# Performance work log

Hardware: AMD Instinct MI355X
Metric: run time of the kernel (lower is better)

## Reference

```python
import jax, jax.numpy as jnp
import numpy as np

B, S, D_X, D_H = 1024, 512, 128, 128
A_VOCAB, A_EMB, T_VOCAB, T_EMB = 100, 32, 4, 16
GRU_IN = D_X + A_EMB + T_EMB + 1  # 177
Y_IN = D_H + D_X + A_EMB + T_EMB  # 304


def _lin_init(key, d_in, d_out):
    k1, k2 = jax.random.split(key)
    lim = 1.0 / np.sqrt(d_in)
    W = jax.random.uniform(k1, (d_out, d_in), minval=-lim, maxval=lim, dtype=jnp.float32)
    b = jax.random.uniform(k2, (d_out,), minval=-lim, maxval=lim, dtype=jnp.float32)
    return W, b


def setup_inputs() -> dict:
    key = jax.random.key(0)
    ks = jax.random.split(key, 16)
    x = jax.random.normal(ks[0], (B, D_X), dtype=jnp.float32)
    a = jax.random.randint(ks[1], (B, S), 0, A_VOCAB)
    t = jax.random.randint(ks[2], (B, S), 0, T_VOCAB)
    y = jax.random.uniform(ks[3], (B, S), dtype=jnp.float32)
    mask = jnp.ones((B, S), dtype=jnp.float32)

    xW, xb = _lin_init(ks[4], D_X, D_X)                 # x_proj
    a_emb = jax.random.normal(ks[5], (A_VOCAB, A_EMB), dtype=jnp.float32)
    t_emb = jax.random.normal(ks[6], (T_VOCAB, T_EMB), dtype=jnp.float32)
    W_ih, b_ih = _lin_init(ks[7], GRU_IN, 3 * D_H)      # GRUCell input weights
    W_hh, b_hh = _lin_init(ks[8], D_H, 3 * D_H)         # GRUCell hidden weights
    h0W, h0b = _lin_init(ks[9], D_X, D_H)               # h0 MLP
    tW1, tb1 = _lin_init(ks[10], D_H, D_H)              # t_head
    tW2, tb2 = _lin_init(ks[11], D_H, T_VOCAB)
    yW1, yb1 = _lin_init(ks[12], Y_IN, D_H)             # y_head
    yW2, yb2 = _lin_init(ks[13], D_H, 1)
    return {
        'x': x, 'a': a, 't': t, 'y': y, 'mask': mask,
        'xW': xW, 'xb': xb, 'a_emb': a_emb, 't_emb': t_emb,
        'W_ih': W_ih, 'b_ih': b_ih, 'W_hh': W_hh, 'b_hh': b_hh,
        'h0W': h0W, 'h0b': h0b,
        'tW1': tW1, 'tb1': tb1, 'tW2': tW2, 'tb2': tb2,
        'yW1': yW1, 'yb1': yb1, 'yW2': yW2, 'yb2': yb2,
    }


def _crn_forward(x, y, mask, xW, xb, a_emb, t_emb, W_ih, b_ih, W_hh, b_hh,
                 h0W, h0b, tW1, tb1, tW2, tb2, yW1, yb1, yW2, yb2, a, t):
    gelu = lambda v: jax.nn.gelu(v, approximate=False)
    x_enc = x @ xW.T + xb                       # [B, D_X]
    h = jnp.tanh(x_enc @ h0W.T + h0b)           # [B, D_H]
    a_e = a_emb[a]                              # [B, S, A_EMB]
    t_e = t_emb[t]                              # [B, S, T_EMB]
    y3 = y[..., None]                           # [B, S, 1]

    # time-major slices for scan
    a_e_t = jnp.swapaxes(a_e, 0, 1)
    t_e_t = jnp.swapaxes(t_e, 0, 1)
    y_t = jnp.swapaxes(y3, 0, 1)
    m_t = jnp.swapaxes(mask, 0, 1)[..., None]   # [S, B, 1]

    def step(h, inp):
        ae, te, yt, m = inp
        # grad_reverse is identity in forward; dropout off (eval)
        t_logits = gelu(h @ tW1.T + tb1) @ tW2.T + tb2          # [B, T_VOCAB]
        y_in = jnp.concatenate([h, x_enc, ae, te], axis=-1)
        y_logits = gelu(y_in @ yW1.T + yb1) @ yW2.T + yb2        # [B, 1]
        upd = jnp.concatenate([x_enc, ae, te, yt], axis=-1)      # [B, GRU_IN]
        gx = upd @ W_ih.T + b_ih
        gh = h @ W_hh.T + b_hh
        r = jax.nn.sigmoid(gx[:, :D_H] + gh[:, :D_H])
        z = jax.nn.sigmoid(gx[:, D_H:2 * D_H] + gh[:, D_H:2 * D_H])
        n = jnp.tanh(gx[:, 2 * D_H:] + r * gh[:, 2 * D_H:])
        h_next = (1.0 - z) * n + z * h
        h_new = m * h_next + (1.0 - m) * h
        return h_new, (y_logits, t_logits, h)

    _, (y_seq, t_seq, h_seq) = jax.lax.scan(step, h, (a_e_t, t_e_t, y_t, m_t))
    # back to batch-major [B, S, ...]
    return (jnp.swapaxes(y_seq, 0, 1), jnp.swapaxes(t_seq, 0, 1), jnp.swapaxes(h_seq, 0, 1))


def reference(x, a, t, y, mask, xW, xb, a_emb, t_emb, W_ih, b_ih, W_hh, b_hh,
              h0W, h0b, tW1, tb1, tW2, tb2, yW1, yb1, yW2, yb2):
    return _crn_forward(x, y, mask, xW, xb, a_emb, t_emb, W_ih, b_ih, W_hh, b_hh,
                        h0W, h0b, tW1, tb1, tW2, tb2, yW1, yb1, yW2, yb2, a, t)
```

## Files before the change

### kernel.cpp

```cpp
#include <hip/hip_runtime.h>
#include <math.h>

#define SLEN 512

typedef _Float16 half8 __attribute__((ext_vector_type(8)));
typedef _Float16 half2v __attribute__((ext_vector_type(2)));
typedef __fp16 fp16x2 __attribute__((ext_vector_type(2)));
typedef float f32x4 __attribute__((ext_vector_type(4)));
typedef unsigned int uint;

union U4H8 { uint4 u; half8 h; };
union UH2 { uint u; half2v v; fp16x2 p; };

static __device__ __forceinline__ uint packh2(float a, float b){
  UH2 x; x.p = __builtin_amdgcn_cvt_pkrtz(a, b); return x.u;
}
static __device__ __forceinline__ float loh(uint u){ UH2 x; x.u=u; return (float)x.v[0]; }
static __device__ __forceinline__ float hih(uint u){ UH2 x; x.u=u; return (float)x.v[1]; }
static __device__ __forceinline__ half8 ld_h8(const uint* p){
  U4H8 x; x.u = *(const uint4*)p; return x.h;
}
static __device__ __forceinline__ float rcpf(float x){ return __builtin_amdgcn_rcpf(x); }
static __device__ __forceinline__ float sigm(float v){ return rcpf(1.0f+__expf(-v)); }
static __device__ __forceinline__ float tanh_f(float v){ return 1.0f - 2.0f*rcpf(__expf(2.0f*v)+1.0f); }
static __device__ __forceinline__ float gelu_exact(float v){
  return 0.5f*v*(1.0f+erff(v*0.7071067811865475f));
}
#define MFMA(a,b,c) __builtin_amdgcn_mfma_f32_16x16x32_f16((a),(b),(c),0,0,0)

static __device__ __forceinline__ void wg_barrier(){
  __builtin_amdgcn_sched_barrier(0);
  asm volatile("s_waitcnt lgkmcnt(0)" ::: "memory");
  __builtin_amdgcn_s_barrier();
  __builtin_amdgcn_sched_barrier(0);
}

__global__ void k_sample(const float* __restrict__ x, const float* __restrict__ xW, const float* __restrict__ xb,
                         const float* __restrict__ h0W, const float* __restrict__ h0b,
                         const float* __restrict__ W_ih, const float* __restrict__ b_ih, const float* __restrict__ b_hh,
                         const float* __restrict__ yW1, const float* __restrict__ yb1,
                         float* __restrict__ w_h0, float* __restrict__ w_xgx, float* __restrict__ w_yx)
{
  const int b = blockIdx.x, tid = threadIdx.x;
  __shared__ float sx[128];
  __shared__ float sxe[128];
  if (tid < 128) sx[tid] = x[b*128+tid];
  __syncthreads();
  if (tid < 128) {
    float acc = xb[tid];
    #pragma unroll 8
    for (int j=0;j<128;++j) acc += xW[tid*128+j]*sx[j];
    sxe[tid] = acc;
  }
  __syncthreads();
  {
    const int o = tid;
    float acc = b_ih[o] + (o < 256 ? b_hh[o] : 0.f);
    #pragma unroll 8
    for (int j=0;j<128;++j) acc += W_ih[o*177+j]*sxe[j];
    w_xgx[b*384+o] = acc;
  }
  if (tid < 128) {
    float acc = h0b[tid];
    #pragma unroll 8
    for (int j=0;j<128;++j) acc += h0W[tid*128+j]*sxe[j];
    w_h0[b*128+tid] = tanhf(acc);
    float a2 = yb1[tid];
    #pragma unroll 8
    for (int j=0;j<128;++j) a2 += yW1[tid*304+128+j]*sxe[j];
    w_yx[b*128+tid] = a2;
  }
}

__global__ __launch_bounds__(384,1) void k_recur(
  const float* __restrict__ W_hh, const float* __restrict__ W_ih, const float* __restrict__ b_hh,
  const int* __restrict__ a, const int* __restrict__ tt,
  const float* __restrict__ yy, const float* __restrict__ mask,
  const float* __restrict__ w_h0, const float* __restrict__ w_xgx,
  const float* __restrict__ a_emb, const float* __restrict__ t_emb,
  float* __restrict__ o_h, uint* __restrict__ h16)
{
  const int tid = threadIdx.x;
  const int wv = tid>>6, lane = tid&63, q = lane>>4, c = lane&15;
  const int g = wv>>1, H = wv&1;
  const int b0 = blockIdx.x*16;
  const int rowbase = g*128 + H*64;

  __shared__ __align__(16) uint s_h[2][16*68];
  __shared__ __align__(16) uint s_ext[2][16*36];
  __shared__ __align__(16) uint s_rz[2][1024];
  __shared__ __align__(16) uint s_chunk[2][1024];
  __shared__ __align__(16) uint s_al[1600];
  __shared__ __align__(16) uint s_te[32];

  half8 wf[24];
  #pragma unroll
  for (int t4=0;t4<4;++t4) {
    const int row = rowbase + t4*16 + c;
    #pragma unroll
    for (int kt=0;kt<4;++kt) {
      const float4* wp = (const float4*)(W_hh + row*128 + kt*32 + q*8);
      float4 v0 = wp[0], v1 = wp[1];
      half8 hv;
      hv[0]=(_Float16)v0.x; hv[1]=(_Float16)v0.y; hv[2]=(_Float16)v0.z; hv[3]=(_Float16)v0.w;
      hv[4]=(_Float16)v1.x; hv[5]=(_Float16)v1.y; hv[6]=(_Float16)v1.z; hv[7]=(_Float16)v1.w;
      wf[t4*6+kt] = hv;
    }
    #pragma unroll
    for (int kt=4;kt<6;++kt) {
      half8 hv;
      #pragma unroll
      for (int j=0;j<8;++j) {
        int k2 = (kt-4)*32 + q*8 + j;
        float v = (k2 < 49) ? W_ih[row*177 + 128 + k2] : 0.f;
        hv[j] = (_Float16)v;
      }
      wf[t4*6+kt] = hv;
    }
  }
  f32x4 xg[4];
  #pragma unroll
  for (int t4=0;t4<4;++t4)
    #pragma unroll
    for (int r=0;r<4;++r)
      xg[t4][r] = w_xgx[(b0+c)*384 + rowbase + t4*16 + q*4 + r];
  f32x4 bhh[4]; float hm[16];
  if (g==2) {
    #pragma unroll
    for (int t4=0;t4<4;++t4)
      #pragma unroll
      for (int r=0;r<4;++r) {
        bhh[t4][r] = b_hh[256 + H*64 + t4*16 + q*4 + r];
        hm[t4*4+r] = w_h0[(b0+c)*128 + H*64 + t4*16 + q*4 + r];
      }
  }
  for (int d = tid; d < 1600; d += 384) {
    int row = d>>4, col = d&15;
    s_al[d] = packh2(a_emb[row*32+2*col], a_emb[row*32+2*col+1]);
  }
  if (tid < 32) {
    int row = tid>>3, col = tid&7;
    s_te[tid] = packh2(t_emb[row*16+2*col], t_emb[row*16+2*col+1]);
  }
  uint4 cr0, cr1, cr2, cr3;
  if (wv==0) {
    const uint* bp = (q==0) ? (const uint*)a : (q==1) ? (const uint*)tt
                   : (q==2) ? (const uint*)yy : (const uint*)mask;
    const uint4* p = (const uint4*)(bp + (size_t)(b0+c)*512);
    cr0=p[0]; cr1=p[1]; cr2=p[2]; cr3=p[3];
    uint4* dst = (uint4*)&s_chunk[0][q*256 + c*16];
    dst[0]=cr0; dst[1]=cr1; dst[2]=cr2; dst[3]=cr3;
  }
  if (g==2) {
    #pragma unroll
    for (int t4=0;t4<4;++t4) {
      int base = c*68 + H*32 + t4*8 + q*2;
      s_h[0][base]   = packh2(hm[t4*4+0], hm[t4*4+1]);
      s_h[0][base+1] = packh2(hm[t4*4+2], hm[t4*4+3]);
    }
  }
  __syncthreads();
  if (g==0) {
    int av = (int)s_chunk[0][c*16];
    int tv = (int)s_chunk[0][256 + c*16];
    uint yu = s_chunk[0][512 + c*16];
    float yv = __uint_as_float(yu);
    #pragma unroll
    for (int i=0;i<4;++i) {
      int d = H*16 + q*4 + i;
      uint u;
      if (d < 16) u = s_al[av*16 + d];
      else if (d < 24) u = s_te[tv*8 + (d-16)];
      else if (d == 24) u = packh2(yv, 0.f);
      else u = 0u;
      s_ext[0][c*36 + d] = u;
    }
  }
  __syncthreads();

  f32x4 acc[4], acc2[4];

  for (int s=0; s<SLEN; ++s) {
    const int pb = s&1;
    half8 hb[4], eb[2];
    #pragma unroll
    for (int kt=0;kt<4;++kt) hb[kt] = ld_h8(&s_h[pb][c*68 + kt*16 + q*4]);
    #pragma unroll
    for (int e=0;e<2;++e)    eb[e]  = ld_h8(&s_ext[pb][c*36 + e*16 + q*4]);

    if (g < 2) {
      if (g==1 && s>0) {
        const int ob = (s-1)&1;
        const int smp = H*8 + (lane>>3), ch = lane&7;
        const uint* hp = &s_h[ob][smp*68 + ch*8];
        const size_t pr = (size_t)(b0+smp)*SLEN + (s-1);
        if (h16) {
          uint4* hq = (uint4*)(h16 + pr*64 + ch*8);
          hq[0] = *(const uint4*)(hp);
          hq[1] = *(const uint4*)(hp + 4);
        } else {
          float* op = o_h + pr*128 + ch*16;
          #pragma unroll
          for (int i2=0;i2<2;++i2) {
            uint4 u = *(const uint4*)(hp + i2*4);
            float4 f0 = make_float4(loh(u.x), hih(u.x), loh(u.y), hih(u.y));
            float4 f1 = make_float4(loh(u.z), hih(u.z), loh(u.w), hih(u.w));
            *(float4*)(op + i2*8)     = f0;
            *(float4*)(op + i2*8 + 4) = f1;
          }
        }
      }
      #pragma unroll
      for (int t4=0;t4<4;++t4) acc[t4] = xg[t4];
      #pragma unroll
      for (int kt=0;kt<6;++kt) {
        half8 bsel = (kt<4) ? hb[kt] : eb[kt-4];
        #pragma unroll
        for (int t4=0;t4<4;++t4) acc[t4] = MFMA(wf[t4*6+kt], bsel, acc[t4]);
      }
      #pragma unroll
      for (int t4=0;t4<4;++t4)
        #pragma unroll
        for (int pr=0;pr<2;++pr) {
          float s0 = sigm(acc[t4][2*pr]), s1 = sigm(acc[t4][2*pr+1]);
          s_rz[g][(((H*4+t4)*2+pr)*4+q)*16 + c] = packh2(s0, s1);
        }
      if (wv==0) {
        if ((s&15)==8 && s<490) {
          const int s0n = ((s>>4)+1)*16;
          const uint* bp = (q==0) ? (const uint*)a : (q==1) ? (const uint*)tt
                         : (q==2) ? (const uint*)yy : (const uint*)mask;
          const uint4* p = (const uint4*)(bp + (size_t)(b0+c)*512 + s0n);
          cr0=p[0]; cr1=p[1]; cr2=p[2]; cr3=p[3];
        }
        if ((s&15)==9 && s<491) {
          uint4* dst = (uint4*)&s_chunk[((s>>4)+1)&1][q*256 + c*16];
          dst[0]=cr0; dst[1]=cr1; dst[2]=cr2; dst[3]=cr3;
        }
      }
    } else {
      #pragma unroll
      for (int t4=0;t4<4;++t4) { acc[t4] = bhh[t4]; acc2[t4] = xg[t4]; }
      #pragma unroll
      for (int kt=0;kt<4;++kt)
        #pragma unroll
        for (int t4=0;t4<4;++t4) acc[t4] = MFMA(wf[t4*6+kt], hb[kt], acc[t4]);
      #pragma unroll
      for (int kt=4;kt<6;++kt)
        #pragma unroll
        for (int t4=0;t4<4;++t4) acc2[t4] = MFMA(wf[t4*6+kt], eb[kt-4], acc2[t4]);
    }
    wg_barrier();
    if (g==2) {
      const float mval = __uint_as_float(s_chunk[(s>>4)&1][768 + c*16 + (s&15)]);
      #pragma unroll
      for (int t4=0;t4<4;++t4)
        #pragma unroll
        for (int pr=0;pr<2;++pr) {
          const int slot = (((H*4+t4)*2+pr)*4+q)*16 + c;
          uint ru = s_rz[0][slot], zu = s_rz[1][slot];
          const int i0 = t4*4 + 2*pr;
          float n0 = tanh_f(acc2[t4][2*pr]   + loh(ru)*acc[t4][2*pr]);
          float n1 = tanh_f(acc2[t4][2*pr+1] + hih(ru)*acc[t4][2*pr+1]);
          float h0o = hm[i0], h1o = hm[i0+1];
          float hn0 = n0 + loh(zu)*(h0o - n0);
          float hn1 = n1 + hih(zu)*(h1o - n1);
          hm[i0]   = h0o + mval*(hn0 - h0o);
          hm[i0+1] = h1o + mval*(hn1 - h1o);
        }
      const int nb = (s+1)&1;
      #pragma unroll
      for (int t4=0;t4<4;++t4) {
        int base = c*68 + H*32 + t4*8 + q*2;
        s_h[nb][base]   = packh2(hm[t4*4+0], hm[t4*4+1]);
        s_h[nb][base+1] = packh2(hm[t4*4+2], hm[t4*4+3]);
      }
    } else if (g==0 && s < SLEN-1) {
      const int sn = s+1;
      const int par2 = (sn>>4)&1, st = sn&15;
      int av = (int)s_chunk[par2][c*16 + st];
      int tv = (int)s_chunk[par2][256 + c*16 + st];
      float yv = __uint_as_float(s_chunk[par2][512 + c*16 + st]);
      #pragma unroll
      for (int i=0;i<4;++i) {
        int d = H*16 + q*4 + i;
        uint u;
        if (d < 16) u = s_al[av*16 + d];
        else if (d < 24) u = s_te[tv*8 + (d-16)];
        else if (d == 24) u = packh2(yv, 0.f);
        else u = 0u;
        s_ext[(s+1)&1][c*36 + d] = u;
      }
    }
    wg_barrier();
  }
  if (g==1) {
    const int ob = (SLEN-1)&1;
    const int smp = H*8 + (lane>>3), ch = lane&7;
    const uint* hp = &s_h[ob][smp*68 + ch*8];
    const size_t pr = (size_t)(b0+smp)*SLEN + (SLEN-1);
    if (h16) {
      uint4* hq = (uint4*)(h16 + pr*64 + ch*8);
      hq[0] = *(const uint4*)(hp);
      hq[1] = *(const uint4*)(hp + 4);
    } else {
      float* op = o_h + pr*128 + ch*16;
      #pragma unroll
      for (int i2=0;i2<2;++i2) {
        uint4 u = *(const uint4*)(hp + i2*4);
        float4 f0 = make_float4(loh(u.x), hih(u.x), loh(u.y), hih(u.y));
        float4 f1 = make_float4(loh(u.z), hih(u.z), loh(u.w), hih(u.w));
        *(float4*)(op + i2*8)     = f0;
        *(float4*)(op + i2*8 + 4) = f1;
      }
    }
  }
}

template<bool H16>
__global__ __launch_bounds__(256,2) void k_heads(
  const float* __restrict__ tW1, const float* __restrict__ tb1,
  const float* __restrict__ tW2, const float* __restrict__ tb2,
  const float* __restrict__ yW1, const float* __restrict__ yW2, const float* __restrict__ yb2,
  const int* __restrict__ a, const int* __restrict__ tt,
  const float* __restrict__ w_yx,
  const float* __restrict__ a_emb, const float* __restrict__ t_emb,
  const float* __restrict__ h_f32, const uint* __restrict__ h16,
  float* __restrict__ o_y, float* __restrict__ o_t, float* __restrict__ o_h)
{
  const int tid = threadIdx.x;
  const int wv = tid>>6, lane = tid&63, q = lane>>4, c = lane&15;
  const bool isY = (wv >= 2);
  const int uh = wv&1;
  const int pair = wv>>1;
  const int p0 = blockIdx.x*1024;
  const int b0 = blockIdx.x*2;

  __shared__ __align__(16) uint s_al[100*20];
  __shared__ __align__(16) uint s_te[32];
  __shared__ __align__(16) uint s_gb[2][2][16*68];

  for (int d = tid; d < 1600; d += 256) {
    int row = d>>4, col = d&15;
    s_al[row*20+col] = packh2(a_emb[row*32+2*col], a_emb[row*32+2*col+1]);
  }
  if (tid < 32) {
    int row = tid>>3, col = tid&7;
    s_te[row*8+col] = packh2(t_emb[row*16+2*col], t_emb[row*16+2*col+1]);
  }

  half8 wf[24];
  const float* W1 = isY ? yW1 : tW1;
  const int w1stride = isY ? 304 : 128;
  #pragma unroll
  for (int ut=0;ut<4;++ut) {
    const int unit = uh*64 + ut*16 + c;
    #pragma unroll
    for (int kt=0;kt<4;++kt) {
      const float4* wp = (const float4*)(W1 + unit*w1stride + kt*32 + q*8);
      float4 v0 = wp[0], v1 = wp[1];
      half8 hv;
      hv[0]=(_Float16)v0.x; hv[1]=(_Float16)v0.y; hv[2]=(_Float16)v0.z; hv[3]=(_Float16)v0.w;
      hv[4]=(_Float16)v1.x; hv[5]=(_Float16)v1.y; hv[6]=(_Float16)v1.z; hv[7]=(_Float16)v1.w;
      wf[ut*6+kt] = hv;
    }
    #pragma unroll
    for (int kt=4;kt<6;++kt) {
      half8 hv;
      #pragma unroll
      for (int j=0;j<8;++j) {
        int k2 = (kt-4)*32 + q*8 + j;
        float v = (isY && k2 < 48) ? yW1[unit*304 + 256 + k2] : 0.f;
        hv[j] = (_Float16)v;
      }
      wf[ut*6+kt] = hv;
    }
  }
  half8 w2f[4];
  #pragma unroll
  for (int kt=0;kt<4;++kt) {
    half8 hv;
    #pragma unroll
    for (int j=0;j<8;++j) {
      float v = 0.f;
      if (!isY && c < 4) v = tW2[c*128 + kt*32 + q*8 + j];
      if ( isY && c == 0) v = yW2[kt*32 + q*8 + j];
      hv[j] = (_Float16)v;
    }
    w2f[kt] = hv;
  }
  float tb2r[4]; float yb2s = yb2[0];
  #pragma unroll
  for (int r=0;r<4;++r) tb2r[r] = tb2[r];

  __syncthreads();

  #pragma unroll 1
  for (int bh=0; bh<2; ++bh) {
    f32x4 bsr[4];
    #pragma unroll
    for (int ut=0;ut<4;++ut)
      #pragma unroll
      for (int r=0;r<4;++r)
        bsr[ut][r] = isY ? w_yx[(b0+bh)*128 + uh*64 + ut*16 + q*4 + r]
                         : tb1[uh*64 + ut*16 + q*4 + r];

    #pragma unroll 1
    for (int ti=0; ti<32; ++ti) {
      const int tile = bh*32 + ti;
      const int par = ti&1;
      const int p = p0 + tile*16 + c;

      half8 hb[4];
      if (H16) {
        const uint* hp = h16 + (size_t)p*64;
        #pragma unroll
        for (int kt=0;kt<4;++kt) hb[kt] = ld_h8(hp + kt*16 + q*4);
      } else {
        const float* hp = h_f32 + (size_t)p*128;
        #pragma unroll
        for (int kt=0;kt<4;++kt) {
          const float4* fp = (const float4*)(hp + kt*32 + q*8);
          float4 v0 = fp[0], v1 = fp[1];
          half8 hv;
          hv[0]=(_Float16)v0.x; hv[1]=(_Float16)v0.y; hv[2]=(_Float16)v0.z; hv[3]=(_Float16)v0.w;
          hv[4]=(_Float16)v1.x; hv[5]=(_Float16)v1.y; hv[6]=(_Float16)v1.z; hv[7]=(_Float16)v1.w;
          hb[kt] = hv;
        }
      }
      if (H16 && !isY) {
        float* op = o_h + (size_t)p*128;
        #pragma unroll
        for (int kk=0;kk<2;++kk) {
          const int kt = uh*2 + kk;
          float4 f0 = make_float4((float)hb[kt][0], (float)hb[kt][1], (float)hb[kt][2], (float)hb[kt][3]);
          float4 f1 = make_float4((float)hb[kt][4], (float)hb[kt][5], (float)hb[kt][6], (float)hb[kt][7]);
          *(float4*)(op + kt*32 + q*8)     = f0;
          *(float4*)(op + kt*32 + q*8 + 4) = f1;
        }
      }

      f32x4 acc[4];
      #pragma unroll
      for (int ut=0;ut<4;++ut) acc[ut] = bsr[ut];
      #pragma unroll
      for (int kt=0;kt<4;++kt)
        #pragma unroll
        for (int ut=0;ut<4;++ut) acc[ut] = MFMA(wf[ut*6+kt], hb[kt], acc[ut]);
      if (isY) {
        half8 eb[2];
        const int av = a[p], tv = tt[p];
        eb[0] = ld_h8(&s_al[av*20 + q*4]);
        if (q < 2) eb[1] = ld_h8(&s_te[tv*8 + q*4]);
        else {
          half8 z;
          #pragma unroll
          for (int j=0;j<8;++j) z[j] = (_Float16)0.f;
          eb[1] = z;
        }
        #pragma unroll
        for (int kt=4;kt<6;++kt)
          #pragma unroll
          for (int ut=0;ut<4;++ut) acc[ut] = MFMA(wf[ut*6+kt], eb[kt-4], acc[ut]);
      }

      #pragma unroll
      for (int ut=0;ut<4;++ut)
        #pragma unroll
        for (int pr=0;pr<2;++pr) {
          float g0 = gelu_exact(acc[ut][2*pr]);
          float g1 = gelu_exact(acc[ut][2*pr+1]);
          s_gb[pair][par][c*68 + uh*32 + ut*8 + 2*q + pr] = packh2(g0, g1);
        }
      wg_barrier();

      f32x4 a2; a2[0]=0.f; a2[1]=0.f; a2[2]=0.f; a2[3]=0.f;
      #pragma unroll
      for (int kt=0;kt<4;++kt) {
        half8 gb = ld_h8(&s_gb[pair][par][c*68 + kt*16 + q*4]);
        a2 = MFMA(w2f[kt], gb, a2);
      }
      if (uh==0 && lane < 16) {
        if (!isY) {
          float4 o = make_float4(a2[0]+tb2r[0], a2[1]+tb2r[1], a2[2]+tb2r[2], a2[3]+tb2r[3]);
          *(float4*)&o_t[(size_t)p*4] = o;
        } else {
          o_y[p] = a2[0] + yb2s;
        }
      }
    }
  }
}

extern "C" void kernel_launch(void* const* d_in, const int* in_sizes, int n_in,
                              void* d_out, int out_size, void* d_ws, size_t ws_size,
                              hipStream_t stream) {
  (void)in_sizes; (void)n_in; (void)out_size;
  const float* x     = (const float*)d_in[0];
  const int*   a     = (const int*)  d_in[1];
  const int*   tt    = (const int*)  d_in[2];
  const float* y     = (const float*)d_in[3];
  const float* mask  = (const float*)d_in[4];
  const float* xW    = (const float*)d_in[5];
  const float* xb    = (const float*)d_in[6];
  const float* a_emb = (const float*)d_in[7];
  const float* t_emb = (const float*)d_in[8];
  const float* W_ih  = (const float*)d_in[9];
  const float* b_ih  = (const float*)d_in[10];
  const float* W_hh  = (const float*)d_in[11];
  const float* b_hh  = (const float*)d_in[12];
  const float* h0W   = (const float*)d_in[13];
  const float* h0b   = (const float*)d_in[14];
  const float* tW1   = (const float*)d_in[15];
  const float* tb1   = (const float*)d_in[16];
  const float* tW2   = (const float*)d_in[17];
  const float* tb2   = (const float*)d_in[18];
  const float* yW1   = (const float*)d_in[19];
  const float* yb1   = (const float*)d_in[20];
  const float* yW2   = (const float*)d_in[21];
  const float* yb2   = (const float*)d_in[22];

  float* o_y = (float*)d_out;
  float* o_t = o_y + 524288;
  float* o_h = o_y + 2621440;

  float* ws    = (float*)d_ws;
  float* w_h0  = ws;
  float* w_xgx = ws + 131072;
  float* w_yx  = ws + 524288;

  const size_t H16_BYTES = (size_t)524288 * 256;
  uint* h16 = nullptr;
  if (ws_size >= (size_t)655360*4 + H16_BYTES) h16 = (uint*)(ws + 655360);

  k_sample<<<1024, 384, 0, stream>>>(x, xW, xb, h0W, h0b, W_ih, b_ih, b_hh, yW1, yb1,
                                     w_h0, w_xgx, w_yx);
  k_recur<<<64, 384, 0, stream>>>(W_hh, W_ih, b_hh, a, tt, y, mask,
                                  w_h0, w_xgx, a_emb, t_emb, o_h, h16);
  if (h16)
    k_heads<true><<<512, 256, 0, stream>>>(tW1, tb1, tW2, tb2, yW1, yW2, yb2, a, tt,
                                           w_yx, a_emb, t_emb, o_h, h16, o_y, o_t, o_h);
  else
    k_heads<false><<<512, 256, 0, stream>>>(tW1, tb1, tW2, tb2, yW1, yW2, yb2, a, tt,
                                            w_yx, a_emb, t_emb, o_h, nullptr, o_y, o_t, o_h);
}
```

Measured before the change: 1.354 ms.

## Restructure GRU recurrence to 8 waves owning all gates per row slice

The recurrent kernel now uses 8 waves, each computing the r, z and n gates for its own 16 hidden units. This removes the cross-wave exchange of r/z through shared memory and drops one of the two workgroup barriers per timestep. Each wave also builds its own embedding input and writes h directly, instead of having dedicated waves prepare the input and store h. The heads kernel is flattened into a single 64-tile loop that prefetches the next tile's h and indices, and the second-layer work alternates between wave halves. The costs are more waves per block and duplicated embedding loads in every wave.

```diff
diff --git a/kernel.cpp b/kernel.cpp
--- a/kernel.cpp
+++ b/kernel.cpp
@@ -28,11 +28,9 @@
 }
 #define MFMA(a,b,c) __builtin_amdgcn_mfma_f32_16x16x32_f16((a),(b),(c),0,0,0)
 
-static __device__ __forceinline__ void wg_barrier(){
-  __builtin_amdgcn_sched_barrier(0);
+static __device__ __forceinline__ void wg_sync(){
   asm volatile("s_waitcnt lgkmcnt(0)" ::: "memory");
   __builtin_amdgcn_s_barrier();
-  __builtin_amdgcn_sched_barrier(0);
 }
 
 __global__ void k_sample(const float* __restrict__ x, const float* __restrict__ xW, const float* __restrict__ xb,
@@ -72,7 +70,7 @@
   }
 }
 
-__global__ __launch_bounds__(384,1) void k_recur(
+__global__ __launch_bounds__(512,1) void k_recur(
   const float* __restrict__ W_hh, const float* __restrict__ W_ih, const float* __restrict__ b_hh,
   const int* __restrict__ a, const int* __restrict__ tt,
   const float* __restrict__ yy, const float* __restrict__ mask,
@@ -82,32 +80,29 @@
 {
   const int tid = threadIdx.x;
   const int wv = tid>>6, lane = tid&63, q = lane>>4, c = lane&15;
-  const int g = wv>>1, H = wv&1;
   const int b0 = blockIdx.x*16;
-  const int rowbase = g*128 + H*64;
+  const int r0 = wv*16;
 
   __shared__ __align__(16) uint s_h[2][16*68];
-  __shared__ __align__(16) uint s_ext[2][16*36];
-  __shared__ __align__(16) uint s_rz[2][1024];
   __shared__ __align__(16) uint s_chunk[2][1024];
   __shared__ __align__(16) uint s_al[1600];
   __shared__ __align__(16) uint s_te[32];
 
-  half8 wf[24];
-  #pragma unroll
-  for (int t4=0;t4<4;++t4) {
-    const int row = rowbase + t4*16 + c;
-    #pragma unroll
-    for (int kt=0;kt<4;++kt) {
+  half8 wf[18];
+  #pragma unroll
+  for (int g=0; g<3; ++g) {
+    const int row = g*128 + r0 + c;
+    #pragma unroll
+    for (int kt=0; kt<4; ++kt) {
       const float4* wp = (const float4*)(W_hh + row*128 + kt*32 + q*8);
       float4 v0 = wp[0], v1 = wp[1];
       half8 hv;
       hv[0]=(_Float16)v0.x; hv[1]=(_Float16)v0.y; hv[2]=(_Float16)v0.z; hv[3]=(_Float16)v0.w;
       hv[4]=(_Float16)v1.x; hv[5]=(_Float16)v1.y; hv[6]=(_Float16)v1.z; hv[7]=(_Float16)v1.w;
-      wf[t4*6+kt] = hv;
-    }
-    #pragma unroll
-    for (int kt=4;kt<6;++kt) {
+      wf[g*6+kt] = hv;
+    }
+    #pragma unroll
+    for (int kt=4; kt<6; ++kt) {
       half8 hv;
       #pragma unroll
       for (int j=0;j<8;++j) {
@@ -115,26 +110,20 @@
         float v = (k2 < 49) ? W_ih[row*177 + 128 + k2] : 0.f;
         hv[j] = (_Float16)v;
       }
-      wf[t4*6+kt] = hv;
-    }
-  }
-  f32x4 xg[4];
-  #pragma unroll
-  for (int t4=0;t4<4;++t4)
-    #pragma unroll
-    for (int r=0;r<4;++r)
-      xg[t4][r] = w_xgx[(b0+c)*384 + rowbase + t4*16 + q*4 + r];
-  f32x4 bhh[4]; float hm[16];
-  if (g==2) {
-    #pragma unroll
-    for (int t4=0;t4<4;++t4)
-      #pragma unroll
-      for (int r=0;r<4;++r) {
-        bhh[t4][r] = b_hh[256 + H*64 + t4*16 + q*4 + r];
-        hm[t4*4+r] = w_h0[(b0+c)*128 + H*64 + t4*16 + q*4 + r];
-      }
-  }
-  for (int d = tid; d < 1600; d += 384) {
+      wf[g*6+kt] = hv;
+    }
+  }
+  f32x4 xgr, xgz, xgn, bhh, hm;
+  #pragma unroll
+  for (int j=0;j<4;++j) {
+    const int rr = r0 + q*4 + j;
+    xgr[j] = w_xgx[(b0+c)*384 +       rr];
+    xgz[j] = w_xgx[(b0+c)*384 + 128 + rr];
+    xgn[j] = w_xgx[(b0+c)*384 + 256 + rr];
+    bhh[j] = b_hh[256 + rr];
+    hm[j]  = w_h0[(b0+c)*128 + rr];
+  }
+  for (int d = tid; d < 1600; d += 512) {
     int row = d>>4, col = d&15;
     s_al[d] = packh2(a_emb[row*32+2*col], a_emb[row*32+2*col+1]);
   }
@@ -151,169 +140,66 @@
     uint4* dst = (uint4*)&s_chunk[0][q*256 + c*16];
     dst[0]=cr0; dst[1]=cr1; dst[2]=cr2; dst[3]=cr3;
   }
-  if (g==2) {
-    #pragma unroll
-    for (int t4=0;t4<4;++t4) {
-      int base = c*68 + H*32 + t4*8 + q*2;
-      s_h[0][base]   = packh2(hm[t4*4+0], hm[t4*4+1]);
-      s_h[0][base+1] = packh2(hm[t4*4+2], hm[t4*4+3]);
-    }
-  }
+  s_h[0][c*68 + wv*8 + q*2]     = packh2(hm[0], hm[1]);
+  s_h[0][c*68 + wv*8 + q*2 + 1] = packh2(hm[2], hm[3]);
   __syncthreads();
-  if (g==0) {
-    int av = (int)s_chunk[0][c*16];
-    int tv = (int)s_chunk[0][256 + c*16];
-    uint yu = s_chunk[0][512 + c*16];
-    float yv = __uint_as_float(yu);
-    #pragma unroll
-    for (int i=0;i<4;++i) {
-      int d = H*16 + q*4 + i;
-      uint u;
-      if (d < 16) u = s_al[av*16 + d];
-      else if (d < 24) u = s_te[tv*8 + (d-16)];
-      else if (d == 24) u = packh2(yv, 0.f);
-      else u = 0u;
-      s_ext[0][c*36 + d] = u;
-    }
-  }
-  __syncthreads();
-
-  f32x4 acc[4], acc2[4];
 
   for (int s=0; s<SLEN; ++s) {
-    const int pb = s&1;
-    half8 hb[4], eb[2];
+    const int pb = s&1, par = (s>>4)&1, st = s&15;
+    half8 hb[4];
     #pragma unroll
     for (int kt=0;kt<4;++kt) hb[kt] = ld_h8(&s_h[pb][c*68 + kt*16 + q*4]);
-    #pragma unroll
-    for (int e=0;e<2;++e)    eb[e]  = ld_h8(&s_ext[pb][c*36 + e*16 + q*4]);
-
-    if (g < 2) {
-      if (g==1 && s>0) {
-        const int ob = (s-1)&1;
-        const int smp = H*8 + (lane>>3), ch = lane&7;
-        const uint* hp = &s_h[ob][smp*68 + ch*8];
-        const size_t pr = (size_t)(b0+smp)*SLEN + (s-1);
-        if (h16) {
-          uint4* hq = (uint4*)(h16 + pr*64 + ch*8);
-          hq[0] = *(const uint4*)(hp);
-          hq[1] = *(const uint4*)(hp + 4);
-        } else {
-          float* op = o_h + pr*128 + ch*16;
-          #pragma unroll
-          for (int i2=0;i2<2;++i2) {
-            uint4 u = *(const uint4*)(hp + i2*4);
-            float4 f0 = make_float4(loh(u.x), hih(u.x), loh(u.y), hih(u.y));
-            float4 f1 = make_float4(loh(u.z), hih(u.z), loh(u.w), hih(u.w));
-            *(float4*)(op + i2*8)     = f0;
-            *(float4*)(op + i2*8 + 4) = f1;
-          }
-        }
-      }
-      #pragma unroll
-      for (int t4=0;t4<4;++t4) acc[t4] = xg[t4];
-      #pragma unroll
-      for (int kt=0;kt<6;++kt) {
-        half8 bsel = (kt<4) ? hb[kt] : eb[kt-4];
-        #pragma unroll
-        for (int t4=0;t4<4;++t4) acc[t4] = MFMA(wf[t4*6+kt], bsel, acc[t4]);
-      }
-      #pragma unroll
-      for (int t4=0;t4<4;++t4)
-        #pragma unroll
-        for (int pr=0;pr<2;++pr) {
-          float s0 = sigm(acc[t4][2*pr]), s1 = sigm(acc[t4][2*pr+1]);
-          s_rz[g][(((H*4+t4)*2+pr)*4+q)*16 + c] = packh2(s0, s1);
-        }
-      if (wv==0) {
-        if ((s&15)==8 && s<490) {
-          const int s0n = ((s>>4)+1)*16;
-          const uint* bp = (q==0) ? (const uint*)a : (q==1) ? (const uint*)tt
-                         : (q==2) ? (const uint*)yy : (const uint*)mask;
-          const uint4* p = (const uint4*)(bp + (size_t)(b0+c)*512 + s0n);
-          cr0=p[0]; cr1=p[1]; cr2=p[2]; cr3=p[3];
-        }
-        if ((s&15)==9 && s<491) {
-          uint4* dst = (uint4*)&s_chunk[((s>>4)+1)&1][q*256 + c*16];
-          dst[0]=cr0; dst[1]=cr1; dst[2]=cr2; dst[3]=cr3;
-        }
-      }
-    } else {
-      #pragma unroll
-      for (int t4=0;t4<4;++t4) { acc[t4] = bhh[t4]; acc2[t4] = xg[t4]; }
-      #pragma unroll
-      for (int kt=0;kt<4;++kt)
-        #pragma unroll
-        for (int t4=0;t4<4;++t4) acc[t4] = MFMA(wf[t4*6+kt], hb[kt], acc[t4]);
-      #pragma unroll
-      for (int kt=4;kt<6;++kt)
-        #pragma unroll
-        for (int t4=0;t4<4;++t4) acc2[t4] = MFMA(wf[t4*6+kt], eb[kt-4], acc2[t4]);
-    }
-    wg_barrier();
-    if (g==2) {
-      const float mval = __uint_as_float(s_chunk[(s>>4)&1][768 + c*16 + (s&15)]);
-      #pragma unroll
-      for (int t4=0;t4<4;++t4)
-        #pragma unroll
-        for (int pr=0;pr<2;++pr) {
-          const int slot = (((H*4+t4)*2+pr)*4+q)*16 + c;
-          uint ru = s_rz[0][slot], zu = s_rz[1][slot];
-          const int i0 = t4*4 + 2*pr;
-          float n0 = tanh_f(acc2[t4][2*pr]   + loh(ru)*acc[t4][2*pr]);
-          float n1 = tanh_f(acc2[t4][2*pr+1] + hih(ru)*acc[t4][2*pr+1]);
-          float h0o = hm[i0], h1o = hm[i0+1];
-          float hn0 = n0 + loh(zu)*(h0o - n0);
-          float hn1 = n1 + hih(zu)*(h1o - n1);
-          hm[i0]   = h0o + mval*(hn0 - h0o);
-          hm[i0+1] = h1o + mval*(hn1 - h1o);
-        }
-      const int nb = (s+1)&1;
-      #pragma unroll
-      for (int t4=0;t4<4;++t4) {
-        int base = c*68 + H*32 + t4*8 + q*2;
-        s_h[nb][base]   = packh2(hm[t4*4+0], hm[t4*4+1]);
-        s_h[nb][base+1] = packh2(hm[t4*4+2], hm[t4*4+3]);
-      }
-    } else if (g==0 && s < SLEN-1) {
-      const int sn = s+1;
-      const int par2 = (sn>>4)&1, st = sn&15;
-      int av = (int)s_chunk[par2][c*16 + st];
-      int tv = (int)s_chunk[par2][256 + c*16 + st];
-      float yv = __uint_as_float(s_chunk[par2][512 + c*16 + st]);
-      #pragma unroll
-      for (int i=0;i<4;++i) {
-        int d = H*16 + q*4 + i;
-        uint u;
-        if (d < 16) u = s_al[av*16 + d];
-        else if (d < 24) u = s_te[tv*8 + (d-16)];
-        else if (d == 24) u = packh2(yv, 0.f);
-        else u = 0u;
-        s_ext[(s+1)&1][c*36 + d] = u;
-      }
-    }
-    wg_barrier();
-  }
-  if (g==1) {
-    const int ob = (SLEN-1)&1;
-    const int smp = H*8 + (lane>>3), ch = lane&7;
-    const uint* hp = &s_h[ob][smp*68 + ch*8];
-    const size_t pr = (size_t)(b0+smp)*SLEN + (SLEN-1);
-    if (h16) {
-      uint4* hq = (uint4*)(h16 + pr*64 + ch*8);
-      hq[0] = *(const uint4*)(hp);
-      hq[1] = *(const uint4*)(hp + 4);
-    } else {
-      float* op = o_h + pr*128 + ch*16;
-      #pragma unroll
-      for (int i2=0;i2<2;++i2) {
-        uint4 u = *(const uint4*)(hp + i2*4);
-        float4 f0 = make_float4(loh(u.x), hih(u.x), loh(u.y), hih(u.y));
-        float4 f1 = make_float4(loh(u.z), hih(u.z), loh(u.w), hih(u.w));
-        *(float4*)(op + i2*8)     = f0;
-        *(float4*)(op + i2*8 + 4) = f1;
-      }
-    }
+    const int av = (int)s_chunk[par][c*16 + st];
+    const int tv = (int)s_chunk[par][256 + c*16 + st];
+    const float yv = __uint_as_float(s_chunk[par][512 + c*16 + st]);
+    const float mval = __uint_as_float(s_chunk[par][768 + c*16 + st]);
+    half8 eb0 = ld_h8(&s_al[av*16 + q*4]);
+    half8 eb1;
+    if (q < 2) eb1 = ld_h8(&s_te[tv*8 + q*4]);
+    else { U4H8 t; t.u = make_uint4((q==2)?packh2(yv,0.f):0u,0u,0u,0u); eb1 = t.h; }
+    {
+      const size_t p = (size_t)(b0+c)*SLEN + s;
+      if (h16) {
+        uint2 u; u.x = packh2(hm[0], hm[1]); u.y = packh2(hm[2], hm[3]);
+        *(uint2*)(h16 + p*64 + wv*8 + q*2) = u;
+      } else {
+        *(float4*)(o_h + p*128 + r0 + q*4) = make_float4(hm[0],hm[1],hm[2],hm[3]);
+      }
+    }
+    f32x4 ar = xgr, az = xgz, anh = bhh, anx = xgn;
+    #pragma unroll
+    for (int kt=0;kt<4;++kt) {
+      ar  = MFMA(wf[kt],      hb[kt], ar);
+      az  = MFMA(wf[6+kt],    hb[kt], az);
+      anh = MFMA(wf[12+kt],   hb[kt], anh);
+    }
+    ar  = MFMA(wf[4],  eb0, ar);   ar  = MFMA(wf[5],  eb1, ar);
+    az  = MFMA(wf[10], eb0, az);   az  = MFMA(wf[11], eb1, az);
+    anx = MFMA(wf[16], eb0, anx);  anx = MFMA(wf[17], eb1, anx);
+    #pragma unroll
+    for (int j=0;j<4;++j) {
+      float rj = sigm(ar[j]), zj = sigm(az[j]);
+      float nj = tanh_f(anx[j] + rj*anh[j]);
+      float hn = nj + zj*(hm[j] - nj);
+      hm[j] = hm[j] + mval*(hn - hm[j]);
+    }
+    const int nb = (s+1)&1;
+    s_h[nb][c*68 + wv*8 + q*2]     = packh2(hm[0], hm[1]);
+    s_h[nb][c*68 + wv*8 + q*2 + 1] = packh2(hm[2], hm[3]);
+    if (wv==0) {
+      if ((st)==8 && s<490) {
+        const int s0n = ((s>>4)+1)*16;
+        const uint* bp = (q==0) ? (const uint*)a : (q==1) ? (const uint*)tt
+                       : (q==2) ? (const uint*)yy : (const uint*)mask;
+        const uint4* p = (const uint4*)(bp + (size_t)(b0+c)*512 + s0n);
+        cr0=p[0]; cr1=p[1]; cr2=p[2]; cr3=p[3];
+      }
+      if ((st)==9 && s<491) {
+        uint4* dst = (uint4*)&s_chunk[((s>>4)+1)&1][q*256 + c*16];
+        dst[0]=cr0; dst[1]=cr1; dst[2]=cr2; dst[3]=cr3;
+      }
+    }
+    wg_sync();
   }
 }
 
@@ -392,95 +278,115 @@
   float tb2r[4]; float yb2s = yb2[0];
   #pragma unroll
   for (int r=0;r<4;++r) tb2r[r] = tb2[r];
+  f32x4 bsr0[4], bsr1[4];
+  #pragma unroll
+  for (int ut=0;ut<4;++ut)
+    #pragma unroll
+    for (int r=0;r<4;++r) {
+      const int u = uh*64 + ut*16 + q*4 + r;
+      bsr0[ut][r] = isY ? w_yx[(b0+0)*128 + u] : tb1[u];
+      bsr1[ut][r] = isY ? w_yx[(b0+1)*128 + u] : tb1[u];
+    }
 
   __syncthreads();
 
+  half8 hbn[4];
+  int avn = 0, tvn = 0;
+  if (H16) {
+    const uint* hp = h16 + (size_t)(p0 + c)*64;
+    #pragma unroll
+    for (int kt=0;kt<4;++kt) hbn[kt] = ld_h8(hp + kt*16 + q*4);
+  }
+  if (isY) { avn = a[p0 + c]; tvn = tt[p0 + c]; }
+
   #pragma unroll 1
-  for (int bh=0; bh<2; ++bh) {
-    f32x4 bsr[4];
+  for (int ti=0; ti<64; ++ti) {
+    const int par = ti&1;
+    const int p = p0 + ti*16 + c;
+
+    half8 hb[4];
+    if (H16) {
+      #pragma unroll
+      for (int kt=0;kt<4;++kt) hb[kt] = hbn[kt];
+    } else {
+      const float* hp = h_f32 + (size_t)p*128;
+      #pragma unroll
+      for (int kt=0;kt<4;++kt) {
+        const float4* fp = (const float4*)(hp + kt*32 + q*8);
+        float4 v0 = fp[0], v1 = fp[1];
+        half8 hv;
+        hv[0]=(_Float16)v0.x; hv[1]=(_Float16)v0.y; hv[2]=(_Float16)v0.z; hv[3]=(_Float16)v0.w;
+        hv[4]=(_Float16)v1.x; hv[5]=(_Float16)v1.y; hv[6]=(_Float16)v1.z; hv[7]=(_Float16)v1.w;
+        hb[kt] = hv;
+      }
+    }
+    const int av = avn, tv = tvn;
+
+    if (H16 && !isY) {
+      float* op = o_h + (size_t)p*128;
+      #pragma unroll
+      for (int kk=0;kk<2;++kk) {
+        const int kt = uh*2 + kk;
+        float4 f0 = make_float4((float)hb[kt][0], (float)hb[kt][1], (float)hb[kt][2], (float)hb[kt][3]);
+        float4 f1 = make_float4((float)hb[kt][4], (float)hb[kt][5], (float)hb[kt][6], (float)hb[kt][7]);
+        *(float4*)(op + kt*32 + q*8)     = f0;
+        *(float4*)(op + kt*32 + q*8 + 4) = f1;
+      }
+    }
+
+    f32x4 acc[4];
+    #pragma unroll
+    for (int ut=0;ut<4;++ut) acc[ut] = (ti < 32) ? bsr0[ut] : bsr1[ut];
+    #pragma unroll
+    for (int kt=0;kt<4;++kt)
+      #pragma unroll
+      for (int ut=0;ut<4;++ut) acc[ut] = MFMA(wf[ut*6+kt], hb[kt], acc[ut]);
+    if (isY) {
+      half8 eb[2];
+      eb[0] = ld_h8(&s_al[av*20 + q*4]);
+      if (q < 2) eb[1] = ld_h8(&s_te[tv*8 + q*4]);
+      else {
+        half8 z;
+        #pragma unroll
+        for (int j=0;j<8;++j) z[j] = (_Float16)0.f;
+        eb[1] = z;
+      }
+      #pragma unroll
+      for (int kt=4;kt<6;++kt)
+        #pragma unroll
+        for (int ut=0;ut<4;++ut) acc[ut] = MFMA(wf[ut*6+kt], eb[kt-4], acc[ut]);
+    }
+
     #pragma unroll
     for (int ut=0;ut<4;++ut)
       #pragma unroll
-      for (int r=0;r<4;++r)
-        bsr[ut][r] = isY ? w_yx[(b0+bh)*128 + uh*64 + ut*16 + q*4 + r]
-                         : tb1[uh*64 + ut*16 + q*4 + r];
-
-    #pragma unroll 1
-    for (int ti=0; ti<32; ++ti) {
-      const int tile = bh*32 + ti;
-      const int par = ti&1;
-      const int p = p0 + tile*16 + c;
-
-      half8 hb[4];
+      for (int pr=0;pr<2;++pr) {
+        float g0 = gelu_exact(acc[ut][2*pr]);
+        float g1 = gelu_exact(acc[ut][2*pr+1]);
+        s_gb[pair][par][c*68 + uh*32 + ut*8 + 2*q + pr] = packh2(g0, g1);
+      }
+
+    {
+      const int tn = (ti < 63) ? ti+1 : 63;
+      const int pn = p0 + tn*16 + c;
       if (H16) {
-        const uint* hp = h16 + (size_t)p*64;
+        const uint* hp = h16 + (size_t)pn*64;
         #pragma unroll
-        for (int kt=0;kt<4;++kt) hb[kt] = ld_h8(hp + kt*16 + q*4);
-      } else {
-        const float* hp = h_f32 + (size_t)p*128;
-        #pragma unroll
-        for (int kt=0;kt<4;++kt) {
-          const float4* fp = (const float4*)(hp + kt*32 + q*8);
-          float4 v0 = fp[0], v1 = fp[1];
-          half8 hv;
-          hv[0]=(_Float16)v0.x; hv[1]=(_Float16)v0.y; hv[2]=(_Float16)v0.z; hv[3]=(_Float16)v0.w;
-          hv[4]=(_Float16)v1.x; hv[5]=(_Float16)v1.y; hv[6]=(_Float16)v1.z; hv[7]=(_Float16)v1.w;
-          hb[kt] = hv;
-        }
-      }
-      if (H16 && !isY) {
-        float* op = o_h + (size_t)p*128;
-        #pragma unroll
-        for (int kk=0;kk<2;++kk) {
-          const int kt = uh*2 + kk;
-          float4 f0 = make_float4((float)hb[kt][0], (float)hb[kt][1], (float)hb[kt][2], (float)hb[kt][3]);
-          float4 f1 = make_float4((float)hb[kt][4], (float)hb[kt][5], (float)hb[kt][6], (float)hb[kt][7]);
-          *(float4*)(op + kt*32 + q*8)     = f0;
-          *(float4*)(op + kt*32 + q*8 + 4) = f1;
-        }
-      }
-
-      f32x4 acc[4];
-      #pragma unroll
-      for (int ut=0;ut<4;++ut) acc[ut] = bsr[ut];
-      #pragma unroll
-      for (int kt=0;kt<4;++kt)
-        #pragma unroll
-        for (int ut=0;ut<4;++ut) acc[ut] = MFMA(wf[ut*6+kt], hb[kt], acc[ut]);
-      if (isY) {
-        half8 eb[2];
-        const int av = a[p], tv = tt[p];
-        eb[0] = ld_h8(&s_al[av*20 + q*4]);
-        if (q < 2) eb[1] = ld_h8(&s_te[tv*8 + q*4]);
-        else {
-          half8 z;
-          #pragma unroll
-          for (int j=0;j<8;++j) z[j] = (_Float16)0.f;
-          eb[1] = z;
-        }
-        #pragma unroll
-        for (int kt=4;kt<6;++kt)
-          #pragma unroll
-          for (int ut=0;ut<4;++ut) acc[ut] = MFMA(wf[ut*6+kt], eb[kt-4], acc[ut]);
-      }
-
-      #pragma unroll
-      for (int ut=0;ut<4;++ut)
-        #pragma unroll
-        for (int pr=0;pr<2;++pr) {
-          float g0 = gelu_exact(acc[ut][2*pr]);
-          float g1 = gelu_exact(acc[ut][2*pr+1]);
-          s_gb[pair][par][c*68 + uh*32 + ut*8 + 2*q + pr] = packh2(g0, g1);
-        }
-      wg_barrier();
-
+        for (int kt=0;kt<4;++kt) hbn[kt] = ld_h8(hp + kt*16 + q*4);
+      }
+      if (isY) { avn = a[pn]; tvn = tt[pn]; }
+    }
+
+    wg_sync();
+
+    if (par == uh) {
       f32x4 a2; a2[0]=0.f; a2[1]=0.f; a2[2]=0.f; a2[3]=0.f;
       #pragma unroll
       for (int kt=0;kt<4;++kt) {
         half8 gb = ld_h8(&s_gb[pair][par][c*68 + kt*16 + q*4]);
         a2 = MFMA(w2f[kt], gb, a2);
       }
-      if (uh==0 && lane < 16) {
+      if (lane < 16) {
         if (!isY) {
           float4 o = make_float4(a2[0]+tb2r[0], a2[1]+tb2r[1], a2[2]+tb2r[2], a2[3]+tb2r[3]);
           *(float4*)&o_t[(size_t)p*4] = o;
@@ -535,7 +441,7 @@
 
   k_sample<<<1024, 384, 0, stream>>>(x, xW, xb, h0W, h0b, W_ih, b_ih, b_hh, yW1, yb1,
                                      w_h0, w_xgx, w_yx);
-  k_recur<<<64, 384, 0, stream>>>(W_hh, W_ih, b_hh, a, tt, y, mask,
+  k_recur<<<64, 512, 0, stream>>>(W_hh, W_ih, b_hh, a, tt, y, mask,
                                   w_h0, w_xgx, a_emb, t_emb, o_h, h16);
   if (h16)
     k_heads<true><<<512, 256, 0, stream>>>(tW1, tb1, tW2, tb2, yW1, yW2, yb2, a, tt,
```

After: 1.194 ms. -11.8%, faster.
